# Performance work log

Measured on AMD Instinct MI355X. Metric: run time of the kernel, lower is better.

## Reference

```python
import jax, jax.numpy as jnp
import numpy as np

B, D, H, R, OUT = 16384, 1024, 4, 1024, 10
LN_EPS = 1e-5


def setup_inputs() -> dict:
    key = jax.random.key(0)
    ks = jax.random.split(key, 20)
    s_in = 1.0 / np.sqrt(D)
    s_hid = 1.0 / np.sqrt(H * R)
    inp = {
        'x': jax.random.normal(ks[0], (B, D), dtype=jnp.float32),
        # block 1
        'wr1': jax.random.normal(ks[1], (H, R, D), dtype=jnp.float32) * s_in,
        'br1': jnp.zeros((H, R), dtype=jnp.float32),
        'wl1': jax.random.normal(ks[2], (H, R, D), dtype=jnp.float32) * s_in,
        'bl1': jnp.zeros((H, R), dtype=jnp.float32),
        'we1': jax.random.normal(ks[3], (D, H * R), dtype=jnp.float32) * s_hid,
        'be1': jnp.zeros((D,), dtype=jnp.float32),
        'g1': jnp.ones((D,), dtype=jnp.float32),
        'b1': jnp.zeros((D,), dtype=jnp.float32),
        # block 2
        'wr2': jax.random.normal(ks[4], (H, R, D), dtype=jnp.float32) * s_in,
        'br2': jnp.zeros((H, R), dtype=jnp.float32),
        'wl2': jax.random.normal(ks[5], (H, R, D), dtype=jnp.float32) * s_in,
        'bl2': jnp.zeros((H, R), dtype=jnp.float32),
        'we2': jax.random.normal(ks[6], (D, H * R), dtype=jnp.float32) * s_hid,
        'be2': jnp.zeros((D,), dtype=jnp.float32),
        'g2': jnp.ones((D,), dtype=jnp.float32),
        'b2': jnp.zeros((D,), dtype=jnp.float32),
        # final linear
        'wf': jax.random.normal(ks[7], (OUT, D), dtype=jnp.float32) * s_in,
        'bf': jnp.zeros((OUT,), dtype=jnp.float32),
    }
    return inp


def _bilinear_block(x, wr, br, wl, bl, we, be):
    # per-basis right/left projections batched into one einsum each: [B,D] x [H,R,D] -> [B,H,R]
    right = jnp.einsum('bd,hrd->bhr', x, wr) + br
    left = jnp.einsum('bd,hrd->bhr', x, wl) + bl
    # elementwise bilinear interaction, concat bases along last dim -> [B, H*R]
    inter = (right * left).reshape(x.shape[0], -1)
    return inter @ we.T + be  # [B, D_out]


def _layernorm(x, g, b):
    mu = jnp.mean(x, axis=-1, keepdims=True)
    var = jnp.mean(jnp.square(x - mu), axis=-1, keepdims=True)
    return (x - mu) * jax.lax.rsqrt(var + LN_EPS) * g + b


def reference(x, wr1, br1, wl1, bl1, we1, be1, g1, b1,
              wr2, br2, wl2, bl2, we2, be2, g2, b2, wf, bf):
    # block 1: bilinear + residual + layernorm
    h = _layernorm(x + _bilinear_block(x, wr1, br1, wl1, bl1, we1, be1), g1, b1)
    # block 2
    h = _layernorm(h + _bilinear_block(h, wr2, br2, wl2, bl2, we2, be2), g2, b2)
    # final linear head
    return h @ wf.T + bf
```

## Files before the change

### kernel.cpp

```cpp
#include <hip/hip_runtime.h>
#include <hip/hip_fp16.h>

#define DEV static __device__ __forceinline__

typedef _Float16 f16;
typedef _Float16 f16x8 __attribute__((ext_vector_type(8)));
typedef _Float16 f16x4 __attribute__((ext_vector_type(4)));
typedef float f32x4 __attribute__((ext_vector_type(4)));

constexpr int BATCH = 16384;
constexpr int D = 1024;
constexpr int HR = 4096;
constexpr int NOUT = 10;

__global__ void k_conv4(const float* __restrict__ s0, f16* __restrict__ d0, int n0,
                        const float* __restrict__ s1, f16* __restrict__ d1, int n1,
                        const float* __restrict__ s2, f16* __restrict__ d2, int n2,
                        const float* __restrict__ s3, f16* __restrict__ d3, int n3) {
    int i = blockIdx.x * blockDim.x + threadIdx.x;
    const int st = gridDim.x * blockDim.x;
    const int tot = n0 + n1 + n2 + n3;
    for (; i < tot; i += st) {
        const float* s; f16* d; int j = i;
        if (j < n0) { s = s0; d = d0; }
        else {
            j -= n0;
            if (j < n1) { s = s1; d = d1; }
            else {
                j -= n1;
                if (j < n2) { s = s2; d = d2; }
                else { j -= n2; s = s3; d = d3; }
            }
        }
        float4 v = reinterpret_cast<const float4*>(s)[j];
        f16x4 h;
        h[0] = (f16)v.x; h[1] = (f16)v.y; h[2] = (f16)v.z; h[3] = (f16)v.w;
        reinterpret_cast<f16x4*>(d)[j] = h;
    }
}

DEV void stage16(void* lds, const void* g) {
    __builtin_amdgcn_global_load_lds(
        (const __attribute__((address_space(1))) void*)g,
        (__attribute__((address_space(3))) void*)lds,
        16, 0, 0);
}

DEV void xcd_map(int bid, int MT, int& mt, int& nt) {
    const int x = bid & 7, q = bid >> 3;
    const int mpx = MT >> 3;
    nt = q / mpx;
    mt = x * mpx + (q % mpx);
}

#define VMCNT(n) asm volatile("s_waitcnt vmcnt(" #n ")" ::: "memory")
#define BAR()    __builtin_amdgcn_s_barrier()
#define PRIO(p)  __builtin_amdgcn_s_setprio(p)

__global__ __launch_bounds__(512, 2) void k_gemm_dual(
    const f16* __restrict__ Xh, const f16* __restrict__ Wr, const f16* __restrict__ Wl,
    const float* __restrict__ br, const float* __restrict__ bl,
    f16* __restrict__ inter, int MT)
{
    extern __shared__ __align__(16) char smem[];
    constexpr int NT = 16;
    constexpr int BUF = 65536;
    constexpr int OA = 0, OR = 32768, OL = 49152;

    int mt, nt;
    xcd_map(blockIdx.x, MT, mt, nt);
    const int m0 = mt * 256, n0 = nt * 128;
    const int tid = threadIdx.x;
    const int lane = tid & 63, wid = tid >> 6;
    const int wm = wid >> 2, wn = wid & 3;
    const int fr = lane & 15, fq = lane >> 4;
    const int xs = (fr & 7) << 4;
    const int dst = tid * 16;

    const int lr = tid >> 3;
    const int cb = ((tid & 7) << 4) ^ ((lr & 7) << 4);
    const char* pA0 = (const char*)Xh + (size_t)(m0 + lr)       * 2048 + cb;
    const char* pA1 = (const char*)Xh + (size_t)(m0 + 128 + lr) * 2048 + cb;
    const char* pA2 = (const char*)Xh + (size_t)(m0 + 64 + lr)  * 2048 + cb;
    const char* pA3 = (const char*)Xh + (size_t)(m0 + 192 + lr) * 2048 + cb;
    const char* pR0 = (const char*)Wr + (size_t)(n0 + lr)       * 2048 + cb;
    const char* pR1 = (const char*)Wr + (size_t)(n0 + 64 + lr)  * 2048 + cb;
    const char* pL0 = (const char*)Wl + (size_t)(n0 + lr)       * 2048 + cb;
    const char* pL1 = (const char*)Wl + (size_t)(n0 + 64 + lr)  * 2048 + cb;

#define D_AOFF(mi,mf,ks) (OA + ((mi)*128 + wm*64 + (mf)*16 + fr)*128 + ((((ks)*64) + fq*16) ^ xs))
#define D_ROFF(nf,ks)    (OR + (wn*32 + (nf)*16 + fr)*128 + ((((ks)*64) + fq*16) ^ xs))
#define D_LOFF(nf,ks)    (OL + (wn*32 + (nf)*16 + fr)*128 + ((((ks)*64) + fq*16) ^ xs))

    f16x8 a[4][2], bR[2][2], bL[2][2];
    f32x4 accR[8][2] = {};
    f32x4 accL[8][2] = {};

    stage16(smem + OA + dst, pA0);          stage16(smem + OA + 8192 + dst, pA1);
    stage16(smem + OR + dst, pR0);          stage16(smem + OR + 8192 + dst, pR1);
    stage16(smem + OL + dst, pL0);          stage16(smem + OL + 8192 + dst, pL1);
    stage16(smem + OA + 16384 + dst, pA2);  stage16(smem + OA + 24576 + dst, pA3);
    VMCNT(4);
    BAR();

    long ko = 128;
    for (int t = 0; t < NT; ++t) {
        char* base = smem + (t & 1) * BUF;
        char* nb   = smem + ((t & 1) ^ 1) * BUF;
        const bool pf = (t + 1) < NT;

#pragma unroll
        for (int mf = 0; mf < 4; ++mf)
#pragma unroll
            for (int ks = 0; ks < 2; ++ks)
                a[mf][ks] = *(const f16x8*)(base + D_AOFF(0, mf, ks));
#pragma unroll
        for (int nf = 0; nf < 2; ++nf)
#pragma unroll
            for (int ks = 0; ks < 2; ++ks)
                bR[nf][ks] = *(const f16x8*)(base + D_ROFF(nf, ks));
        if (pf) { stage16(nb + OA + dst, pA0 + ko); stage16(nb + OA + 8192 + dst, pA1 + ko); }
        PRIO(1);
#pragma unroll
        for (int mf = 0; mf < 4; ++mf)
#pragma unroll
            for (int nf = 0; nf < 2; ++nf)
#pragma unroll
                for (int ks = 0; ks < 2; ++ks)
                    accR[mf][nf] = __builtin_amdgcn_mfma_f32_16x16x32_f16(a[mf][ks], bR[nf][ks], accR[mf][nf], 0, 0, 0);
        PRIO(0);
        if (pf) { VMCNT(4); } else { VMCNT(2); }
        BAR();

#pragma unroll
        for (int nf = 0; nf < 2; ++nf)
#pragma unroll
            for (int ks = 0; ks < 2; ++ks)
                bL[nf][ks] = *(const f16x8*)(base + D_LOFF(nf, ks));
        if (pf) { stage16(nb + OR + dst, pR0 + ko); stage16(nb + OR + 8192 + dst, pR1 + ko); }
        PRIO(1);
#pragma unroll
        for (int mf = 0; mf < 4; ++mf)
#pragma unroll
            for (int nf = 0; nf < 2; ++nf)
#pragma unroll
                for (int ks = 0; ks < 2; ++ks)
                    accL[mf][nf] = __builtin_amdgcn_mfma_f32_16x16x32_f16(a[mf][ks], bL[nf][ks], accL[mf][nf], 0, 0, 0);
        PRIO(0);
        if (pf) { VMCNT(4); } else { VMCNT(0); }
        BAR();

#pragma unroll
        for (int mf = 0; mf < 4; ++mf)
#pragma unroll
            for (int ks = 0; ks < 2; ++ks)
                a[mf][ks] = *(const f16x8*)(base + D_AOFF(1, mf, ks));
        if (pf) { stage16(nb + OL + dst, pL0 + ko); stage16(nb + OL + 8192 + dst, pL1 + ko); }
        PRIO(1);
#pragma unroll
        for (int mf = 0; mf < 4; ++mf)
#pragma unroll
            for (int nf = 0; nf < 2; ++nf)
#pragma unroll
                for (int ks = 0; ks < 2; ++ks)
                    accR[4 + mf][nf] = __builtin_amdgcn_mfma_f32_16x16x32_f16(a[mf][ks], bR[nf][ks], accR[4 + mf][nf], 0, 0, 0);
        PRIO(0);
        BAR();

        if (pf) { stage16(nb + OA + 16384 + dst, pA2 + ko); stage16(nb + OA + 24576 + dst, pA3 + ko); }
        PRIO(1);
#pragma unroll
        for (int mf = 0; mf < 4; ++mf)
#pragma unroll
            for (int nf = 0; nf < 2; ++nf)
#pragma unroll
                for (int ks = 0; ks < 2; ++ks)
                    accL[4 + mf][nf] = __builtin_amdgcn_mfma_f32_16x16x32_f16(a[mf][ks], bL[nf][ks], accL[4 + mf][nf], 0, 0, 0);
        PRIO(0);
        if (pf) { VMCNT(4); }
        BAR();

        ko += 128;
    }

#pragma unroll
    for (int nf = 0; nf < 2; ++nf) {
        const int gc = n0 + wn * 32 + nf * 16 + fr;
        const float brv = br[gc], blv = bl[gc];
#pragma unroll
        for (int mi = 0; mi < 2; ++mi)
#pragma unroll
            for (int mf = 0; mf < 4; ++mf) {
                const int gr0 = m0 + wm * 128 + mi * 64 + mf * 16 + fq * 4;
#pragma unroll
                for (int j = 0; j < 4; ++j) {
                    const float rv = accR[mi * 4 + mf][nf][j] + brv;
                    const float lv = accL[mi * 4 + mf][nf][j] + blv;
                    inter[(size_t)(gr0 + j) * HR + gc] = (f16)(rv * lv);
                }
            }
    }
#undef D_AOFF
#undef D_ROFF
#undef D_LOFF
}

template <typename TR>
DEV void expand_body(const f16* Ain, const f16* Wt, const float* be,
                     const TR* resid, f16* E, int MT)
{
    extern __shared__ __align__(16) char smem[];
    constexpr int NT = 64;
    constexpr int BUF = 65536;
    constexpr int OA = 0, OB = 32768;

    int mt, nt;
    xcd_map(blockIdx.x, MT, mt, nt);
    const int m0 = mt * 256, n0 = nt * 256;
    const int tid = threadIdx.x;
    const int lane = tid & 63, wid = tid >> 6;
    const int wm = wid >> 2, wn = wid & 3;
    const int fr = lane & 15, fq = lane >> 4;
    const int xs = (fr & 7) << 4;
    const int dst = tid * 16;

    const int lr = tid >> 3;
    const int cb = ((tid & 7) << 4) ^ ((lr & 7) << 4);
    const char* pA0 = (const char*)Ain + (size_t)(m0 + lr)       * 8192 + cb;
    const char* pA1 = (const char*)Ain + (size_t)(m0 + 128 + lr) * 8192 + cb;
    const char* pA2 = (const char*)Ain + (size_t)(m0 + 64 + lr)  * 8192 + cb;
    const char* pA3 = (const char*)Ain + (size_t)(m0 + 192 + lr) * 8192 + cb;
    const int r5 = lr & 31, wn2 = lr >> 5;
    const char* pB0 = (const char*)Wt + (size_t)(n0 + wn2 * 64 + r5)        * 8192 + cb;
    const char* pB1 = (const char*)Wt + (size_t)(n0 + (2 + wn2) * 64 + r5)  * 8192 + cb;
    const char* pB2 = (const char*)Wt + (size_t)(n0 + wn2 * 64 + 32 + r5)       * 8192 + cb;
    const char* pB3 = (const char*)Wt + (size_t)(n0 + (2 + wn2) * 64 + 32 + r5) * 8192 + cb;

#define E_AOFF(mi,mf,ks) (OA + ((mi)*128 + wm*64 + (mf)*16 + fr)*128 + ((((ks)*64) + fq*16) ^ xs))
#define E_BOFF(ni,nf,ks) (OB + ((ni)*128 + wn*32 + (nf)*16 + fr)*128 + ((((ks)*64) + fq*16) ^ xs))

    f16x8 a[4][2], b0[2][2], b1[2][2];
    f32x4 acc[8][4] = {};

    stage16(smem + OA + dst, pA0);          stage16(smem + OA + 8192 + dst, pA1);
    stage16(smem + OB + dst, pB0);          stage16(smem + OB + 8192 + dst, pB1);
    stage16(smem + OB + 16384 + dst, pB2);  stage16(smem + OB + 24576 + dst, pB3);
    stage16(smem + OA + 16384 + dst, pA2);  stage16(smem + OA + 24576 + dst, pA3);
    VMCNT(4);
    BAR();

    long ko = 128;
    for (int t = 0; t < NT; ++t) {
        char* base = smem + (t & 1) * BUF;
        char* nb   = smem + ((t & 1) ^ 1) * BUF;
        const bool pf = (t + 1) < NT;

#pragma unroll
        for (int mf = 0; mf < 4; ++mf)
#pragma unroll
            for (int ks = 0; ks < 2; ++ks)
                a[mf][ks] = *(const f16x8*)(base + E_AOFF(0, mf, ks));
#pragma unroll
        for (int nf = 0; nf < 2; ++nf)
#pragma unroll
            for (int ks = 0; ks < 2; ++ks)
                b0[nf][ks] = *(const f16x8*)(base + E_BOFF(0, nf, ks));
        if (pf) { stage16(nb + OA + dst, pA0 + ko); stage16(nb + OA + 8192 + dst, pA1 + ko); }
        PRIO(1);
#pragma unroll
        for (int mf = 0; mf < 4; ++mf)
#pragma unroll
            for (int nf = 0; nf < 2; ++nf)
#pragma unroll
                for (int ks = 0; ks < 2; ++ks)
                    acc[mf][nf] = __builtin_amdgcn_mfma_f32_16x16x32_f16(a[mf][ks], b0[nf][ks], acc[mf][nf], 0, 0, 0);
        PRIO(0);
        if (pf) { VMCNT(4); } else { VMCNT(2); }
        BAR();

#pragma unroll
        for (int nf = 0; nf < 2; ++nf)
#pragma unroll
            for (int ks = 0; ks < 2; ++ks)
                b1[nf][ks] = *(const f16x8*)(base + E_BOFF(1, nf, ks));
        if (pf) { stage16(nb + OB + dst, pB0 + ko); stage16(nb + OB + 8192 + dst, pB1 + ko); }
        PRIO(1);
#pragma unroll
        for (int mf = 0; mf < 4; ++mf)
#pragma unroll
            for (int nf = 0; nf < 2; ++nf)
#pragma unroll
                for (int ks = 0; ks < 2; ++ks)
                    acc[mf][2 + nf] = __builtin_amdgcn_mfma_f32_16x16x32_f16(a[mf][ks], b1[nf][ks], acc[mf][2 + nf], 0, 0, 0);
        PRIO(0);
        if (pf) { VMCNT(4); } else { VMCNT(0); }
        BAR();

#pragma unroll
        for (int mf = 0; mf < 4; ++mf)
#pragma unroll
            for (int ks = 0; ks < 2; ++ks)
                a[mf][ks] = *(const f16x8*)(base + E_AOFF(1, mf, ks));
        if (pf) { stage16(nb + OB + 16384 + dst, pB2 + ko); stage16(nb + OB + 24576 + dst, pB3 + ko); }
        PRIO(1);
#pragma unroll
        for (int mf = 0; mf < 4; ++mf)
#pragma unroll
            for (int nf = 0; nf < 2; ++nf)
#pragma unroll
                for (int ks = 0; ks < 2; ++ks)
                    acc[4 + mf][nf] = __builtin_amdgcn_mfma_f32_16x16x32_f16(a[mf][ks], b0[nf][ks], acc[4 + mf][nf], 0, 0, 0);
        PRIO(0);
        BAR();

        if (pf) { stage16(nb + OA + 16384 + dst, pA2 + ko); stage16(nb + OA + 24576 + dst, pA3 + ko); }
        PRIO(1);
#pragma unroll
        for (int mf = 0; mf < 4; ++mf)
#pragma unroll
            for (int nf = 0; nf < 2; ++nf)
#pragma unroll
                for (int ks = 0; ks < 2; ++ks)
                    acc[4 + mf][2 + nf] = __builtin_amdgcn_mfma_f32_16x16x32_f16(a[mf][ks], b1[nf][ks], acc[4 + mf][2 + nf], 0, 0, 0);
        PRIO(0);
        if (pf) { VMCNT(4); }
        BAR();

        ko += 128;
    }

#pragma unroll
    for (int ni = 0; ni < 2; ++ni)
#pragma unroll
        for (int nf = 0; nf < 2; ++nf) {
            const int gc = n0 + wn * 64 + ni * 32 + nf * 16 + fr;
            const float bev = be[gc];
#pragma unroll
            for (int mi = 0; mi < 2; ++mi)
#pragma unroll
                for (int mf = 0; mf < 4; ++mf) {
                    const int gr0 = m0 + wm * 128 + mi * 64 + mf * 16 + fq * 4;
#pragma unroll
                    for (int j = 0; j < 4; ++j) {
                        const float rv = (float)resid[(size_t)(gr0 + j) * D + gc];
                        E[(size_t)(gr0 + j) * D + gc] = (f16)(acc[mi * 4 + mf][ni * 2 + nf][j] + bev + rv);
                    }
                }
        }
#undef E_AOFF
#undef E_BOFF
}

__global__ __launch_bounds__(512, 2) void k_gemm_expand_f32r(
    const f16* __restrict__ Ain, const f16* __restrict__ Wt,
    const float* __restrict__ be, const float* __restrict__ resid,
    f16* __restrict__ E, int MT)
{ expand_body<float>(Ain, Wt, be, resid, E, MT); }

__global__ __launch_bounds__(512, 2) void k_gemm_expand_f16r(
    const f16* __restrict__ Ain, const f16* __restrict__ Wt,
    const float* __restrict__ be, const f16* __restrict__ resid,
    f16* __restrict__ E, int MT)
{ expand_body<f16>(Ain, Wt, be, resid, E, MT); }

__global__ __launch_bounds__(256) void k_ln(
    f16* __restrict__ EH, const float* __restrict__ g, const float* __restrict__ bb)
{
    const int wid = threadIdx.x >> 6, lane = threadIdx.x & 63;
    const int row = blockIdx.x * 4 + wid;
    f16* er = EH + (size_t)row * D;
    float v[16];
    float s = 0.f, sq = 0.f;
#pragma unroll
    for (int k = 0; k < 16; ++k) {
        const int c = lane + 64 * k;
        v[k] = (float)er[c];
        s += v[k];
        sq += v[k] * v[k];
    }
#pragma unroll
    for (int off = 32; off; off >>= 1) {
        s += __shfl_down(s, off);
        sq += __shfl_down(sq, off);
    }
    s = __shfl(s, 0);
    sq = __shfl(sq, 0);
    const float mu = s * (1.0f / D);
    const float var = sq * (1.0f / D) - mu * mu;
    const float rs = rsqrtf(var + 1e-5f);
#pragma unroll
    for (int k = 0; k < 16; ++k) {
        const int c = lane + 64 * k;
        const float o = (v[k] - mu) * rs * g[c] + bb[c];
        er[c] = (f16)o;
    }
}

__global__ __launch_bounds__(256) void k_ln_head(
    const f16* __restrict__ EH, const float* __restrict__ g, const float* __restrict__ bb,
    const float* __restrict__ Wf, const float* __restrict__ bf, float* __restrict__ outp)
{
    __shared__ float wfs[NOUT * D];
    for (int i = threadIdx.x; i < NOUT * D; i += 256) wfs[i] = Wf[i];
    __syncthreads();
    const int wid = threadIdx.x >> 6, lane = threadIdx.x & 63;
    const int row = blockIdx.x * 4 + wid;
    const f16* er = EH + (size_t)row * D;
    float v[16];
    float s = 0.f, sq = 0.f;
#pragma unroll
    for (int k = 0; k < 16; ++k) {
        const int c = lane + 64 * k;
        v[k] = (float)er[c];
        s += v[k];
        sq += v[k] * v[k];
    }
#pragma unroll
    for (int off = 32; off; off >>= 1) {
        s += __shfl_down(s, off);
        sq += __shfl_down(sq, off);
    }
    s = __shfl(s, 0);
    sq = __shfl(sq, 0);
    const float mu = s * (1.0f / D);
    const float var = sq * (1.0f / D) - mu * mu;
    const float rs = rsqrtf(var + 1e-5f);
#pragma unroll
    for (int k = 0; k < 16; ++k) {
        const int c = lane + 64 * k;
        v[k] = (v[k] - mu) * rs * g[c] + bb[c];
    }
#pragma unroll
    for (int j = 0; j < NOUT; ++j) {
        float p = 0.f;
#pragma unroll
        for (int k = 0; k < 16; ++k) p += v[k] * wfs[j * D + lane + 64 * k];
#pragma unroll
        for (int off = 32; off; off >>= 1) p += __shfl_down(p, off);
        if (lane == 0) outp[(size_t)row * NOUT + j] = p + bf[j];
    }
}

extern "C" void kernel_launch(void* const* d_in, const int* in_sizes, int n_in,
                              void* d_out, int out_size, void* d_ws, size_t ws_size,
                              hipStream_t stream) {
    (void)in_sizes; (void)n_in; (void)out_size;
    const float* x   = (const float*)d_in[0];
    const float* wr1 = (const float*)d_in[1];
    const float* br1 = (const float*)d_in[2];
    const float* wl1 = (const float*)d_in[3];
    const float* bl1 = (const float*)d_in[4];
    const float* we1 = (const float*)d_in[5];
    const float* be1 = (const float*)d_in[6];
    const float* g1  = (const float*)d_in[7];
    const float* b1  = (const float*)d_in[8];
    const float* wr2 = (const float*)d_in[9];
    const float* br2 = (const float*)d_in[10];
    const float* wl2 = (const float*)d_in[11];
    const float* bl2 = (const float*)d_in[12];
    const float* we2 = (const float*)d_in[13];
    const float* be2 = (const float*)d_in[14];
    const float* g2  = (const float*)d_in[15];
    const float* b2  = (const float*)d_in[16];
    const float* wf  = (const float*)d_in[17];
    const float* bf  = (const float*)d_in[18];
    float* outp = (float*)d_out;

    constexpr size_t SZ_W16 = (size_t)HR * D * sizeof(f16);
    constexpr size_t SZ_A16 = (size_t)BATCH * D * sizeof(f16);
    constexpr int SMEM = 2 * 65536;

    hipFuncSetAttribute((const void*)k_gemm_dual,        hipFuncAttributeMaxDynamicSharedMemorySize, SMEM);
    hipFuncSetAttribute((const void*)k_gemm_expand_f32r, hipFuncAttributeMaxDynamicSharedMemorySize, SMEM);
    hipFuncSetAttribute((const void*)k_gemm_expand_f16r, hipFuncAttributeMaxDynamicSharedMemorySize, SMEM);

    char* p = (char*)d_ws;
    f16* wrh = (f16*)p; p += SZ_W16;
    f16* wlh = (f16*)p; p += SZ_W16;
    f16* weh = (f16*)p; p += SZ_W16;
    f16* xh  = (f16*)p; p += SZ_A16;
    f16* EH  = (f16*)p; p += SZ_A16;
    f16* interh = (f16*)p;
    const size_t base = (size_t)(p - (char*)d_ws);
    const size_t avail = ws_size > base ? ws_size - base : 0;

    int CH = 2048;
    if ((size_t)16384 * HR * sizeof(f16) <= avail) CH = 16384;
    else if ((size_t)8192 * HR * sizeof(f16) <= avail) CH = 8192;
    else if ((size_t)4096 * HR * sizeof(f16) <= avail) CH = 4096;

    const int nch = BATCH / CH;
    const int MT = CH / 256;
    const int gDual = MT * (HR / 128);
    const int gExp  = MT * (D / 256);

    constexpr int NW4 = HR * D / 4;
    k_conv4<<<2048, 256, 0, stream>>>(x, xh, BATCH * D / 4,
                                      wr1, wrh, NW4, wl1, wlh, NW4, we1, weh, NW4);

    for (int c = 0; c < nch; ++c) {
        k_gemm_dual<<<gDual, 512, SMEM, stream>>>(xh + (size_t)c * CH * D, wrh, wlh, br1, bl1, interh, MT);
        k_gemm_expand_f32r<<<gExp, 512, SMEM, stream>>>(interh, weh, be1, x + (size_t)c * CH * D,
                                                        EH + (size_t)c * CH * D, MT);
    }
    k_ln<<<BATCH / 4, 256, 0, stream>>>(EH, g1, b1);

    k_conv4<<<1536, 256, 0, stream>>>(wr2, wrh, NW4, wl2, wlh, NW4, we2, weh, NW4,
                                      nullptr, nullptr, 0);

    for (int c = 0; c < nch; ++c) {
        k_gemm_dual<<<gDual, 512, SMEM, stream>>>(EH + (size_t)c * CH * D, wrh, wlh, br2, bl2, interh, MT);
        k_gemm_expand_f16r<<<gExp, 512, SMEM, stream>>>(interh, weh, be2, EH + (size_t)c * CH * D,
                                                        EH + (size_t)c * CH * D, MT);
    }

    k_ln_head<<<BATCH / 4, 256, 0, stream>>>(EH, g2, b2, wf, bf, outp);
}
```

Before: 788.2 us.

## Restructure dual GEMM to 4 waves with larger per-wave tiles

```diff
diff --git a/kernel.cpp b/kernel.cpp
--- a/kernel.cpp
+++ b/kernel.cpp
@@ -57,7 +57,7 @@
 #define BAR()    __builtin_amdgcn_s_barrier()
 #define PRIO(p)  __builtin_amdgcn_s_setprio(p)
 
-__global__ __launch_bounds__(512, 2) void k_gemm_dual(
+__global__ __launch_bounds__(256, 1) void k_gemm_dual(
     const f16* __restrict__ Xh, const f16* __restrict__ Wr, const f16* __restrict__ Wl,
     const float* __restrict__ br, const float* __restrict__ bl,
     f16* __restrict__ inter, int MT)
@@ -72,34 +72,44 @@
     const int m0 = mt * 256, n0 = nt * 128;
     const int tid = threadIdx.x;
     const int lane = tid & 63, wid = tid >> 6;
-    const int wm = wid >> 2, wn = wid & 3;
+    const int wm = wid >> 1, wn = wid & 1;
     const int fr = lane & 15, fq = lane >> 4;
     const int xs = (fr & 7) << 4;
     const int dst = tid * 16;
 
-    const int lr = tid >> 3;
-    const int cb = ((tid & 7) << 4) ^ ((lr & 7) << 4);
-    const char* pA0 = (const char*)Xh + (size_t)(m0 + lr)       * 2048 + cb;
-    const char* pA1 = (const char*)Xh + (size_t)(m0 + 128 + lr) * 2048 + cb;
-    const char* pA2 = (const char*)Xh + (size_t)(m0 + 64 + lr)  * 2048 + cb;
-    const char* pA3 = (const char*)Xh + (size_t)(m0 + 192 + lr) * 2048 + cb;
-    const char* pR0 = (const char*)Wr + (size_t)(n0 + lr)       * 2048 + cb;
-    const char* pR1 = (const char*)Wr + (size_t)(n0 + 64 + lr)  * 2048 + cb;
-    const char* pL0 = (const char*)Wl + (size_t)(n0 + lr)       * 2048 + cb;
-    const char* pL1 = (const char*)Wl + (size_t)(n0 + 64 + lr)  * 2048 + cb;
-
-#define D_AOFF(mi,mf,ks) (OA + ((mi)*128 + wm*64 + (mf)*16 + fr)*128 + ((((ks)*64) + fq*16) ^ xs))
-#define D_ROFF(nf,ks)    (OR + (wn*32 + (nf)*16 + fr)*128 + ((((ks)*64) + fq*16) ^ xs))
-#define D_LOFF(nf,ks)    (OL + (wn*32 + (nf)*16 + fr)*128 + ((((ks)*64) + fq*16) ^ xs))
-
-    f16x8 a[4][2], bR[2][2], bL[2][2];
-    f32x4 accR[8][2] = {};
-    f32x4 accL[8][2] = {};
-
-    stage16(smem + OA + dst, pA0);          stage16(smem + OA + 8192 + dst, pA1);
-    stage16(smem + OR + dst, pR0);          stage16(smem + OR + 8192 + dst, pR1);
-    stage16(smem + OL + dst, pL0);          stage16(smem + OL + 8192 + dst, pL1);
-    stage16(smem + OA + 16384 + dst, pA2);  stage16(smem + OA + 24576 + dst, pA3);
+    const int lr8 = tid >> 3;
+    const int cb = ((tid & 7) << 4) ^ ((lr8 & 7) << 4);
+    const char* pA = (const char*)Xh + (size_t)(m0 + lr8) * 2048 + cb;
+    const char* pR = (const char*)Wr + (size_t)(n0 + lr8) * 2048 + cb;
+    const char* pL = (const char*)Wl + (size_t)(n0 + lr8) * 2048 + cb;
+
+#define D_AOFF(mi,mf,ks) (OA + ((wm)*128 + (mi)*64 + (mf)*16 + fr)*128 + ((((ks)*64) + fq*16) ^ xs))
+#define D_BOFF(o,nf,ks)  ((o) + ((wn)*64 + (nf)*16 + fr)*128 + ((((ks)*64) + fq*16) ^ xs))
+#define STG_A(buf,ko) do { \
+    stage16((buf) + OA + 0     + dst, pA + 0      + (ko)); \
+    stage16((buf) + OA + 4096  + dst, pA + 65536  + (ko)); \
+    stage16((buf) + OA + 16384 + dst, pA + 262144 + (ko)); \
+    stage16((buf) + OA + 20480 + dst, pA + 327680 + (ko)); \
+    stage16((buf) + OA + 8192  + dst, pA + 131072 + (ko)); \
+    stage16((buf) + OA + 12288 + dst, pA + 196608 + (ko)); \
+    stage16((buf) + OA + 24576 + dst, pA + 393216 + (ko)); \
+    stage16((buf) + OA + 28672 + dst, pA + 458752 + (ko)); } while (0)
+#define STG_RL(buf,ko) do { \
+    stage16((buf) + OR + 0     + dst, pR + 0      + (ko)); \
+    stage16((buf) + OR + 4096  + dst, pR + 65536  + (ko)); \
+    stage16((buf) + OR + 8192  + dst, pR + 131072 + (ko)); \
+    stage16((buf) + OR + 12288 + dst, pR + 196608 + (ko)); \
+    stage16((buf) + OL + 0     + dst, pL + 0      + (ko)); \
+    stage16((buf) + OL + 4096  + dst, pL + 65536  + (ko)); \
+    stage16((buf) + OL + 8192  + dst, pL + 131072 + (ko)); \
+    stage16((buf) + OL + 12288 + dst, pL + 196608 + (ko)); } while (0)
+
+    f16x8 a[4][2], bR[4][2], bL[4][2];
+    f32x4 accR[8][4] = {};
+    f32x4 accL[8][4] = {};
+
+    STG_RL(smem, 0);
+    STG_A(smem, 0);
     VMCNT(4);
     BAR();
 
@@ -115,39 +125,25 @@
             for (int ks = 0; ks < 2; ++ks)
                 a[mf][ks] = *(const f16x8*)(base + D_AOFF(0, mf, ks));
 #pragma unroll
-        for (int nf = 0; nf < 2; ++nf)
-#pragma unroll
-            for (int ks = 0; ks < 2; ++ks)
-                bR[nf][ks] = *(const f16x8*)(base + D_ROFF(nf, ks));
-        if (pf) { stage16(nb + OA + dst, pA0 + ko); stage16(nb + OA + 8192 + dst, pA1 + ko); }
+        for (int nf = 0; nf < 4; ++nf)
+#pragma unroll
+            for (int ks = 0; ks < 2; ++ks) {
+                bR[nf][ks] = *(const f16x8*)(base + D_BOFF(OR, nf, ks));
+                bL[nf][ks] = *(const f16x8*)(base + D_BOFF(OL, nf, ks));
+            }
+        if (pf) STG_RL(nb, ko);
         PRIO(1);
 #pragma unroll
         for (int mf = 0; mf < 4; ++mf)
 #pragma unroll
-            for (int nf = 0; nf < 2; ++nf)
-#pragma unroll
-                for (int ks = 0; ks < 2; ++ks)
+            for (int nf = 0; nf < 4; ++nf)
+#pragma unroll
+                for (int ks = 0; ks < 2; ++ks) {
                     accR[mf][nf] = __builtin_amdgcn_mfma_f32_16x16x32_f16(a[mf][ks], bR[nf][ks], accR[mf][nf], 0, 0, 0);
+                    accL[mf][nf] = __builtin_amdgcn_mfma_f32_16x16x32_f16(a[mf][ks], bL[nf][ks], accL[mf][nf], 0, 0, 0);
+                }
         PRIO(0);
-        if (pf) { VMCNT(4); } else { VMCNT(2); }
-        BAR();
-
-#pragma unroll
-        for (int nf = 0; nf < 2; ++nf)
-#pragma unroll
-            for (int ks = 0; ks < 2; ++ks)
-                bL[nf][ks] = *(const f16x8*)(base + D_LOFF(nf, ks));
-        if (pf) { stage16(nb + OR + dst, pR0 + ko); stage16(nb + OR + 8192 + dst, pR1 + ko); }
-        PRIO(1);
-#pragma unroll
-        for (int mf = 0; mf < 4; ++mf)
-#pragma unroll
-            for (int nf = 0; nf < 2; ++nf)
-#pragma unroll
-                for (int ks = 0; ks < 2; ++ks)
-                    accL[mf][nf] = __builtin_amdgcn_mfma_f32_16x16x32_f16(a[mf][ks], bL[nf][ks], accL[mf][nf], 0, 0, 0);
-        PRIO(0);
-        if (pf) { VMCNT(4); } else { VMCNT(0); }
+        if (pf) { VMCNT(8); } else { VMCNT(0); }
         BAR();
 
 #pragma unroll
@@ -155,27 +151,17 @@
 #pragma unroll
             for (int ks = 0; ks < 2; ++ks)
                 a[mf][ks] = *(const f16x8*)(base + D_AOFF(1, mf, ks));
-        if (pf) { stage16(nb + OL + dst, pL0 + ko); stage16(nb + OL + 8192 + dst, pL1 + ko); }
+        if (pf) STG_A(nb, ko);
         PRIO(1);
 #pragma unroll
         for (int mf = 0; mf < 4; ++mf)
 #pragma unroll
-            for (int nf = 0; nf < 2; ++nf)
-#pragma unroll
-                for (int ks = 0; ks < 2; ++ks)
+            for (int nf = 0; nf < 4; ++nf)
+#pragma unroll
+                for (int ks = 0; ks < 2; ++ks) {
                     accR[4 + mf][nf] = __builtin_amdgcn_mfma_f32_16x16x32_f16(a[mf][ks], bR[nf][ks], accR[4 + mf][nf], 0, 0, 0);
-        PRIO(0);
-        BAR();
-
-        if (pf) { stage16(nb + OA + 16384 + dst, pA2 + ko); stage16(nb + OA + 24576 + dst, pA3 + ko); }
-        PRIO(1);
-#pragma unroll
-        for (int mf = 0; mf < 4; ++mf)
-#pragma unroll
-            for (int nf = 0; nf < 2; ++nf)
-#pragma unroll
-                for (int ks = 0; ks < 2; ++ks)
                     accL[4 + mf][nf] = __builtin_amdgcn_mfma_f32_16x16x32_f16(a[mf][ks], bL[nf][ks], accL[4 + mf][nf], 0, 0, 0);
+                }
         PRIO(0);
         if (pf) { VMCNT(4); }
         BAR();
@@ -184,8 +170,8 @@
     }
 
 #pragma unroll
-    for (int nf = 0; nf < 2; ++nf) {
-        const int gc = n0 + wn * 32 + nf * 16 + fr;
+    for (int nf = 0; nf < 4; ++nf) {
+        const int gc = n0 + wn * 64 + nf * 16 + fr;
         const float brv = br[gc], blv = bl[gc];
 #pragma unroll
         for (int mi = 0; mi < 2; ++mi)
@@ -201,8 +187,9 @@
             }
     }
 #undef D_AOFF
-#undef D_ROFF
-#undef D_LOFF
+#undef D_BOFF
+#undef STG_A
+#undef STG_RL
 }
 
 template <typename TR>
@@ -499,7 +486,7 @@
                                       wr1, wrh, NW4, wl1, wlh, NW4, we1, weh, NW4);
 
     for (int c = 0; c < nch; ++c) {
-        k_gemm_dual<<<gDual, 512, SMEM, stream>>>(xh + (size_t)c * CH * D, wrh, wlh, br1, bl1, interh, MT);
+        k_gemm_dual<<<gDual, 256, SMEM, stream>>>(xh + (size_t)c * CH * D, wrh, wlh, br1, bl1, interh, MT);
         k_gemm_expand_f32r<<<gExp, 512, SMEM, stream>>>(interh, weh, be1, x + (size_t)c * CH * D,
                                                         EH + (size_t)c * CH * D, MT);
     }
@@ -509,7 +496,7 @@
                                       nullptr, nullptr, 0);
 
     for (int c = 0; c < nch; ++c) {
-        k_gemm_dual<<<gDual, 512, SMEM, stream>>>(EH + (size_t)c * CH * D, wrh, wlh, br2, bl2, interh, MT);
+        k_gemm_dual<<<gDual, 256, SMEM, stream>>>(EH + (size_t)c * CH * D, wrh, wlh, br2, bl2, interh, MT);
         k_gemm_expand_f16r<<<gExp, 512, SMEM, stream>>>(interh, weh, be2, EH + (size_t)c * CH * D,
                                                         EH + (size_t)c * CH * D, MT);
     }
```

Measured after the change: 880.0 us. +11.6%, slower.
